# Kernel tuning notes

Hardware: AMD Instinct MI355X
Metric: run time of the kernel (lower is better)

The kernel has to match this reference:

```python
import jax, jax.numpy as jnp
import numpy as np

N = 197          # tokens (== token_count)
B = 64           # batch
D = 768          # d_model
NH = 12          # n_head
GH = 2           # global_heads
HR = NH // GH    # head_ratio = 6
DH = 64          # d_head
QK = GH * DH     # qk_dim = 128
ML = 3           # mask_levels
EPS = 1e-5


def setup_inputs() -> dict:
    key = jax.random.key(0)
    ks = jax.random.split(key, 9)
    s = 1.0 / np.sqrt(D)
    return {
        "h": jax.random.normal(ks[0], (N, B, D), dtype=jnp.float32),
        "masks": jax.random.uniform(ks[1], (N, N, ML), dtype=jnp.float32),
        "Wq": jax.random.normal(ks[2], (QK, D), dtype=jnp.float32) * s,
        "Wk": jax.random.normal(ks[3], (QK, D), dtype=jnp.float32) * s,
        "Wv": jax.random.normal(ks[4], (NH * DH, D), dtype=jnp.float32) * s,
        "Wo": jax.random.normal(ks[5], (D, NH * DH), dtype=jnp.float32) * s,
        "mask_proj": jnp.ones((ML, NH), dtype=jnp.float32),
        "ln_gamma": jnp.ones((D,), dtype=jnp.float32),
        "ln_beta": jnp.zeros((D,), dtype=jnp.float32),
    }


def reference(h, masks, Wq, Wk, Wv, Wo, mask_proj, ln_gamma, ln_beta):
    scale = 1.0 / np.sqrt(DH)
    # projections (seq-first layout [N, B, ...])
    q = (h @ Wq.T).reshape(N, B, GH, DH)
    k = (h @ Wk.T).reshape(N, B, GH, DH)
    v = (h @ Wv.T).reshape(N, B, NH, DH)
    # global-head scores: [B, GH, i, j]
    score = jnp.einsum('ibgd,jbgd->bgij', q, k) * scale
    # learned mask mix: [i, j, NH] -> [GH, i, j, HR] (g-major head split, matches torch reshape)
    mw = jnp.einsum('ijl,ln->ijn', masks, mask_proj)
    mw = mw.reshape(N, N, GH, HR).transpose(2, 0, 1, 3)
    # broadcast each global head to HR local heads: [B, GH, i, j, HR]
    attn = score[..., None] * mw[None]
    attn = attn.transpose(0, 1, 4, 2, 3).reshape(B, NH, N, N)  # head = g*HR + r
    prob = jax.nn.softmax(attn, axis=-1)
    # AV: [i, B, NH, DH] -> [N, B, NH*DH]
    vec = jnp.einsum('bnij,jbnd->ibnd', prob, v).reshape(N, B, NH * DH)
    out = vec @ Wo.T
    # post-LN residual
    x = h + out
    mu = jnp.mean(x, axis=-1, keepdims=True)
    var = jnp.var(x, axis=-1, keepdims=True)
    return ln_gamma * (x - mu) / jnp.sqrt(var + EPS) + ln_beta
```

## Files before the change

kernel.cpp:

```cpp
#include <hip/hip_runtime.h>
#include <hip/hip_bf16.h>
#include <stdint.h>

#define NTOK 197
#define NPAD 224
#define BATCH 64
#define DMODEL 768
#define NHEAD 12
#define GHEAD 2
#define HRATIO 6
#define DHEAD 64
#define QKDIM 128
#define LNEPS 1e-5f
#define MROWS (NTOK * BATCH)
#define MPAD 12672

using f32x4 = __attribute__((ext_vector_type(4))) float;
using s16x8 = __attribute__((ext_vector_type(8))) short;
using s16x4 = __attribute__((ext_vector_type(4))) short;

__device__ __forceinline__ short f2bf(float f) {
  unsigned int x = __float_as_uint(f);
  return (short)((x + 0x7fffu + ((x >> 16) & 1u)) >> 16);
}

__device__ __forceinline__ void gld16(void* lds, const void* g) {
  __builtin_amdgcn_global_load_lds(
      (const __attribute__((address_space(1))) unsigned int*)g,
      (__attribute__((address_space(3))) unsigned int*)lds, 16, 0, 0);
}

#define NB_H 4728
#define NB_QKV 384
#define NB_WO 288
__global__ __launch_bounds__(256)
void prep_kernel(const float* __restrict__ h, const float* __restrict__ Wq,
                 const float* __restrict__ Wk, const float* __restrict__ Wv,
                 const float* __restrict__ Wo, short* __restrict__ hb,
                 short* __restrict__ Wqkvb, short* __restrict__ Wob) {
  const int bb = blockIdx.x, t = threadIdx.x;
  const float* src;
  short* dst;
  if (bb < NB_H) {
    int idx = bb * 256 + t;
    src = h + (size_t)idx * 8;
    dst = hb + (size_t)idx * 8;
  } else if (bb < NB_H + NB_QKV) {
    int idx = (bb - NB_H) * 256 + t;
    int r = idx / 96, u = idx - r * 96;
    const float* s0 = (r < 128) ? Wq + (size_t)r * DMODEL
                    : (r < 256) ? Wk + (size_t)(r - 128) * DMODEL
                                : Wv + (size_t)(r - 256) * DMODEL;
    src = s0 + u * 8;
    dst = Wqkvb + (size_t)r * DMODEL + u * 8;
  } else {
    int idx = (bb - NB_H - NB_QKV) * 256 + t;
    src = Wo + (size_t)idx * 8;
    dst = Wob + (size_t)idx * 8;
  }
  float4 a = *(const float4*)src;
  float4 c = *(const float4*)(src + 4);
  s16x8 o;
  o[0] = f2bf(a.x); o[1] = f2bf(a.y); o[2] = f2bf(a.z); o[3] = f2bf(a.w);
  o[4] = f2bf(c.x); o[5] = f2bf(c.y); o[6] = f2bf(c.z); o[7] = f2bf(c.w);
  *(s16x8*)dst = o;
}

template<int OUTMODE>
__global__ __launch_bounds__(256)
void gemm_bt_kernel(const short* __restrict__ A, const short* __restrict__ W,
                    const float* __restrict__ R, void* __restrict__ Cout,
                    int M, int K, int NC) {
  __shared__ short As[128 * 32];
  __shared__ short Ws[128 * 32];
  const int tid = threadIdx.x;
  const int bn = blockIdx.x * 128;
  const int bm = blockIdx.y * 128;
  const int w = tid >> 6, l = tid & 63;
  const int wr = w >> 1, wc = w & 1;
  const int lm = l & 15, lh = l >> 4;

  const int srow = tid >> 2;
  const int schunk = (tid & 3) ^ ((tid >> 3) & 3);
  const short* Ag = A + (size_t)(bm + srow) * K + schunk * 8;
  const short* Wg = W + (size_t)(bn + srow) * K + schunk * 8;

  const int csw = lh ^ ((lm >> 1) & 3);
  f32x4 acc[4][4] = {};

  for (int kt = 0; kt < K; kt += 32) {
    __syncthreads();
    gld16(As + tid * 8, Ag + kt);
    gld16(As + 2048 + tid * 8, Ag + (size_t)64 * K + kt);
    gld16(Ws + tid * 8, Wg + kt);
    gld16(Ws + 2048 + tid * 8, Wg + (size_t)64 * K + kt);
    __syncthreads();
    s16x8 af[4], bf[4];
#pragma unroll
    for (int m = 0; m < 4; ++m)
      af[m] = *(const s16x8*)((const char*)As + (wr * 64 + m * 16 + lm) * 64 + csw * 16);
#pragma unroll
    for (int n = 0; n < 4; ++n)
      bf[n] = *(const s16x8*)((const char*)Ws + (wc * 64 + n * 16 + lm) * 64 + csw * 16);
#pragma unroll
    for (int m = 0; m < 4; ++m)
#pragma unroll
      for (int n = 0; n < 4; ++n)
        acc[m][n] = __builtin_amdgcn_mfma_f32_16x16x32_bf16(af[m], bf[n], acc[m][n], 0, 0, 0);
  }

#pragma unroll
  for (int m = 0; m < 4; ++m) {
#pragma unroll
    for (int r = 0; r < 4; ++r) {
      int row = bm + wr * 64 + m * 16 + lh * 4 + r;
      if (row < M) {
        if (OUTMODE == 0) {
          short* Cb = (short*)Cout;
#pragma unroll
          for (int n = 0; n < 4; ++n) {
            int col = bn + wc * 64 + n * 16 + lm;
            Cb[(size_t)row * NC + col] = f2bf(acc[m][n][r]);
          }
        } else {
          float* Cf = (float*)Cout;
#pragma unroll
          for (int n = 0; n < 4; ++n) {
            int col = bn + wc * 64 + n * 16 + lm;
            size_t idx = (size_t)row * NC + col;
            Cf[idx] = acc[m][n][r] + R[idx];
          }
        }
      }
    }
  }
}

__global__ __launch_bounds__(256)
void packall_kernel(const short* __restrict__ Cb, const float* __restrict__ masks,
                    const float* __restrict__ mproj, short* __restrict__ qp,
                    short* __restrict__ kp, short* __restrict__ vT,
                    float* __restrict__ mwp) {
  __shared__ short Vs[NPAD][DHEAD + 1];
  const int bb = blockIdx.x, t = threadIdx.x;
  if (bb < 256) {
    int b = bb >> 2, g = (bb >> 1) & 1, which = bb & 1;
    short* dst = (which ? kp : qp) + ((size_t)b * GHEAD + g) * NPAD * 64;
    int d = t & 63, iofs = t >> 6;
    for (int i0 = 0; i0 < NPAD; i0 += 4) {
      int i = i0 + iofs;
      short v = 0;
      if (i < NTOK)
        v = Cb[(size_t)(i * BATCH + b) * 1024 + which * QKDIM + g * DHEAD + d];
      int dd = which ? ((((d >> 3) ^ (i & 7)) << 3) | (d & 7)) : d;
      dst[i * 64 + dd] = v;
    }
  } else if (bb < 1024) {
    int vv = bb - 256;
    int b = vv / 12, n = vv - b * 12;
    int d = t & 63, iofs = t >> 6;
    for (int i0 = 0; i0 < NPAD; i0 += 4) {
      int i = i0 + iofs;
      short v = 0;
      if (i < NTOK)
        v = Cb[(size_t)(i * BATCH + b) * 1024 + 256 + n * DHEAD + d];
      Vs[i][d] = v;
    }
    __syncthreads();
    short* dst = vT + ((size_t)b * NHEAD + n) * DHEAD * NPAD;
    int sub = t & 63, dr = t >> 6;
    for (int d0 = 0; d0 < DHEAD; d0 += 4) {
      if (sub < 56) {
        int dd = d0 + dr, j0 = sub * 4;
        s16x4 o;
        o[0] = Vs[j0][dd]; o[1] = Vs[j0 + 1][dd];
        o[2] = Vs[j0 + 2][dd]; o[3] = Vs[j0 + 3][dd];
        *(s16x4*)(dst + dd * NPAD + j0) = o;
      }
    }
  } else {
    int e = (bb - 1024) * 256 + t;
    int n = e >> 12;
    int rem = e & 4095;
    int i = rem >> 4, lm = rem & 15;
    float p0 = mproj[n], p1 = mproj[NHEAD + n], p2 = mproj[2 * NHEAD + n];
    float vals[16];
#pragma unroll
    for (int jf = 0; jf < 16; ++jf) vals[jf] = 0.f;
    if (i < NTOK) {
#pragma unroll
      for (int jf = 0; jf < 14; ++jf) {
        int col = jf * 16 + lm;
        if (col < NTOK) {
          const float* mp = masks + ((size_t)i * NTOK + col) * 3;
          vals[jf] = 0.125f * (mp[0] * p0 + mp[1] * p1 + mp[2] * p2);
        }
      }
    }
    float* dst = mwp + (size_t)e * 16;
#pragma unroll
    for (int q = 0; q < 4; ++q) {
      float4 o = make_float4(vals[q * 4], vals[q * 4 + 1], vals[q * 4 + 2], vals[q * 4 + 3]);
      *(float4*)(dst + q * 4) = o;
    }
  }
}

__global__ __launch_bounds__(256, 2)
void attn_fused_kernel(const short* __restrict__ qp, const short* __restrict__ kp,
                       const short* __restrict__ vT, const float* __restrict__ mwp,
                       short* __restrict__ vec_b) {
  const int it = blockIdx.x, b = blockIdx.y, g = blockIdx.z;
  __shared__ short Ks[NPAD * 64];
  __shared__ short Pt[64 * 256];
  __shared__ float rsb[64];
  const int t = threadIdx.x, w = t >> 6, l = t & 63;
  const int lm = l & 15, lh = l >> 4, l7 = l & 7;

  const short* qg = qp + ((size_t)b * GHEAD + g) * NPAD * 64;
  const short* kg = kp + ((size_t)b * GHEAD + g) * NPAD * 64;

#pragma unroll
  for (int s = 0; s < 7; ++s)
    gld16(Ks + s * 2048 + t * 8, kg + s * 2048 + t * 8);
  int qrow = it * 64 + w * 16 + lm;
  if (qrow > NPAD - 1) qrow = NPAD - 1;
  s16x8 a0 = *(const s16x8*)(qg + qrow * 64 + lh * 8);
  s16x8 a1 = *(const s16x8*)(qg + qrow * 64 + 32 + lh * 8);
  __syncthreads();

  f32x4 acc[14] = {};
#pragma unroll
  for (int jf = 0; jf < 14; ++jf) {
    s16x8 kf0 = *(const s16x8*)((const char*)Ks + (jf * 16 + lm) * 128 + ((lh ^ l7) << 4));
    s16x8 kf1 = *(const s16x8*)((const char*)Ks + (jf * 16 + lm) * 128 + (((4 + lh) ^ l7) << 4));
    acc[jf] = __builtin_amdgcn_mfma_f32_16x16x32_bf16(a0, kf0, acc[jf], 0, 0, 0);
    acc[jf] = __builtin_amdgcn_mfma_f32_16x16x32_bf16(a1, kf1, acc[jf], 0, 0, 0);
  }

  for (int hh = 0; hh < HRATIO; ++hh) {
    const int n = g * HRATIO + hh;
    const short* vg = vT + ((size_t)b * NHEAD + n) * 64 * NPAD;
    s16x8 vf[7];
#pragma unroll
    for (int ks = 0; ks < 7; ++ks)
      vf[ks] = *(const s16x8*)(vg + (w * 16 + lm) * NPAD + ks * 32 + lh * 8);

#pragma unroll
    for (int r = 0; r < 4; ++r) {
      const int row = w * 16 + lh * 4 + r;
      const int i = it * 64 + row;
      const float* mr = mwp + (((size_t)n * 256 + i) * 16 + lm) * 16;
      f32x4 mv0 = *(const f32x4*)(mr);
      f32x4 mv1 = *(const f32x4*)(mr + 4);
      f32x4 mv2 = *(const f32x4*)(mr + 8);
      f32x4 mv3 = *(const f32x4*)(mr + 12);
      float sum = 0.f;
#pragma unroll
      for (int jf = 0; jf < 13; ++jf) {
        float mwv = (jf < 4) ? mv0[jf] : (jf < 8) ? mv1[jf - 4]
                  : (jf < 12) ? mv2[jf - 8] : mv3[jf - 12];
        float pe = __expf(acc[jf][r] * mwv);
        if (jf == 12 && lm >= 5) pe = 0.f;
        sum += pe;
        int byteoff = row * 512 + (((2 * jf + (lm >> 3)) ^ (row & 7)) << 4) + (lm & 7) * 2;
        *(short*)((char*)Pt + byteoff) = f2bf(pe);
      }
      {
        int byteoff = row * 512 + (((26 + (lm >> 3)) ^ (row & 7)) << 4) + (lm & 7) * 2;
        *(short*)((char*)Pt + byteoff) = 0;
      }
#pragma unroll
      for (int off = 8; off; off >>= 1) sum += __shfl_xor(sum, off);
      if (lm == 0) rsb[row] = 1.f / sum;
    }
    __syncthreads();

    __builtin_amdgcn_s_setprio(1);
    f32x4 oacc[4] = {};
#pragma unroll
    for (int fi = 0; fi < 4; ++fi)
#pragma unroll
      for (int ks = 0; ks < 7; ++ks) {
        s16x8 pa = *(const s16x8*)((const char*)Pt + (fi * 16 + lm) * 512 +
                                   (((ks * 4 + lh) ^ l7) << 4));
        oacc[fi] = __builtin_amdgcn_mfma_f32_16x16x32_bf16(pa, vf[ks], oacc[fi], 0, 0, 0);
      }
    __builtin_amdgcn_s_setprio(0);
#pragma unroll
    for (int fi = 0; fi < 4; ++fi)
#pragma unroll
      for (int r = 0; r < 4; ++r) {
        int ia = it * 64 + fi * 16 + lh * 4 + r;
        if (ia < NTOK) {
          float rsv = rsb[fi * 16 + lh * 4 + r];
          vec_b[((size_t)ia * BATCH + b) * DMODEL + n * 64 + w * 16 + lm] =
              f2bf(oacc[fi][r] * rsv);
        }
      }
    __syncthreads();
  }
}

__global__ __launch_bounds__(256)
void ln_kernel(float* __restrict__ x, const float* __restrict__ gamma,
               const float* __restrict__ beta) {
  const int m = blockIdx.x;
  float* row = x + (size_t)m * DMODEL;
  const int tid = threadIdx.x;
  float v0 = row[tid], v1 = row[tid + 256], v2 = row[tid + 512];
  float s = v0 + v1 + v2;
  float sq = v0 * v0 + v1 * v1 + v2 * v2;
#pragma unroll
  for (int off = 32; off; off >>= 1) {
    s += __shfl_xor(s, off);
    sq += __shfl_xor(sq, off);
  }
  __shared__ float ss[4], ssq[4];
  const int w = tid >> 6, lane = tid & 63;
  if (lane == 0) { ss[w] = s; ssq[w] = sq; }
  __syncthreads();
  s = ss[0] + ss[1] + ss[2] + ss[3];
  sq = ssq[0] + ssq[1] + ssq[2] + ssq[3];
  const float inv = 1.0f / (float)DMODEL;
  float mu = s * inv;
  float var = sq * inv - mu * mu;
  float rstd = rsqrtf(var + LNEPS);
  row[tid] = gamma[tid] * (v0 - mu) * rstd + beta[tid];
  row[tid + 256] = gamma[tid + 256] * (v1 - mu) * rstd + beta[tid + 256];
  row[tid + 512] = gamma[tid + 512] * (v2 - mu) * rstd + beta[tid + 512];
}

extern "C" void kernel_launch(void* const* d_in, const int* in_sizes, int n_in,
                              void* d_out, int out_size, void* d_ws, size_t ws_size,
                              hipStream_t stream) {
  const float* h     = (const float*)d_in[0];
  const float* masks = (const float*)d_in[1];
  const float* Wq    = (const float*)d_in[2];
  const float* Wk    = (const float*)d_in[3];
  const float* Wv    = (const float*)d_in[4];
  const float* Wo    = (const float*)d_in[5];
  const float* mproj = (const float*)d_in[6];
  const float* gamma = (const float*)d_in[7];
  const float* beta  = (const float*)d_in[8];
  float* out = (float*)d_out;

  char* ws = (char*)d_ws;
  size_t o = 0;
  auto alloc = [&](size_t bytes) { size_t r = o; o += (bytes + 255) & ~(size_t)255; return r; };
  short* hb    = (short*)(ws + alloc((size_t)MPAD * DMODEL * 2));
  short* Cb    = (short*)(ws + alloc((size_t)MPAD * 1024 * 2));
  short* Wqkvb = (short*)(ws + alloc((size_t)1024 * DMODEL * 2));
  short* Wob   = (short*)(ws + alloc((size_t)DMODEL * DMODEL * 2));
  short* qp    = (short*)(ws + alloc((size_t)BATCH * GHEAD * NPAD * DHEAD * 2));
  short* kp    = (short*)(ws + alloc((size_t)BATCH * GHEAD * NPAD * DHEAD * 2));
  short* vT    = (short*)(ws + alloc((size_t)BATCH * NHEAD * DHEAD * NPAD * 2));
  float* mwp   = (float*)(ws + alloc((size_t)NHEAD * 256 * 16 * 16 * 4));
  short* vec_b = hb;

  prep_kernel<<<NB_H + NB_QKV + NB_WO, 256, 0, stream>>>(h, Wq, Wk, Wv, Wo, hb, Wqkvb, Wob);
  gemm_bt_kernel<0><<<dim3(1024 / 128, MPAD / 128), 256, 0, stream>>>(
      hb, Wqkvb, nullptr, Cb, MROWS, DMODEL, 1024);
  packall_kernel<<<1216, 256, 0, stream>>>(Cb, masks, mproj, qp, kp, vT, mwp);
  attn_fused_kernel<<<dim3(4, BATCH, GHEAD), 256, 0, stream>>>(qp, kp, vT, mwp, vec_b);
  gemm_bt_kernel<1><<<dim3(DMODEL / 128, MPAD / 128), 256, 0, stream>>>(
      vec_b, Wob, h, out, MROWS, DMODEL, DMODEL);
  ln_kernel<<<MROWS, 256, 0, stream>>>(out, gamma, beta);
}
```

Measured before the change: 166.8 us.

## Write output projection as bf16 and fuse residual add into LayerNorm; remap GEMM blocks per XCD

After: 156.0 us. 1.07x faster.

```diff
diff --git a/kernel.cpp b/kernel.cpp
--- a/kernel.cpp
+++ b/kernel.cpp
@@ -22,6 +22,10 @@
 __device__ __forceinline__ short f2bf(float f) {
   unsigned int x = __float_as_uint(f);
   return (short)((x + 0x7fffu + ((x >> 16) & 1u)) >> 16);
+}
+
+__device__ __forceinline__ float bf2f(short s) {
+  return __uint_as_float((unsigned)(unsigned short)s << 16);
 }
 
 __device__ __forceinline__ void gld16(void* lds, const void* g) {
@@ -66,16 +70,21 @@
   *(s16x8*)dst = o;
 }
 
-template<int OUTMODE>
 __global__ __launch_bounds__(256)
 void gemm_bt_kernel(const short* __restrict__ A, const short* __restrict__ W,
-                    const float* __restrict__ R, void* __restrict__ Cout,
-                    int M, int K, int NC) {
+                    short* __restrict__ Cout, int M, int K, int NC) {
   __shared__ short As[128 * 32];
   __shared__ short Ws[128 * 32];
   const int tid = threadIdx.x;
-  const int bn = blockIdx.x * 128;
-  const int bm = blockIdx.y * 128;
+
+  const int nwg = gridDim.x * gridDim.y;
+  const int orig = blockIdx.y * gridDim.x + blockIdx.x;
+  const int qq = nwg >> 3, rr = nwg & 7;
+  const int xcd = orig & 7, sidx = orig >> 3;
+  const int wg = (xcd < rr ? xcd * (qq + 1) : rr * (qq + 1) + (xcd - rr) * qq) + sidx;
+  const int bn = (wg % gridDim.x) * 128;
+  const int bm = (wg / gridDim.x) * 128;
+
   const int w = tid >> 6, l = tid & 63;
   const int wr = w >> 1, wc = w & 1;
   const int lm = l & 15, lh = l >> 4;
@@ -115,21 +124,10 @@
     for (int r = 0; r < 4; ++r) {
       int row = bm + wr * 64 + m * 16 + lh * 4 + r;
       if (row < M) {
-        if (OUTMODE == 0) {
-          short* Cb = (short*)Cout;
-#pragma unroll
-          for (int n = 0; n < 4; ++n) {
-            int col = bn + wc * 64 + n * 16 + lm;
-            Cb[(size_t)row * NC + col] = f2bf(acc[m][n][r]);
-          }
-        } else {
-          float* Cf = (float*)Cout;
-#pragma unroll
-          for (int n = 0; n < 4; ++n) {
-            int col = bn + wc * 64 + n * 16 + lm;
-            size_t idx = (size_t)row * NC + col;
-            Cf[idx] = acc[m][n][r] + R[idx];
-          }
+#pragma unroll
+        for (int n = 0; n < 4; ++n) {
+          int col = bn + wc * 64 + n * 16 + lm;
+          Cout[(size_t)row * NC + col] = f2bf(acc[m][n][r]);
         }
       }
     }
@@ -303,12 +301,17 @@
 }
 
 __global__ __launch_bounds__(256)
-void ln_kernel(float* __restrict__ x, const float* __restrict__ gamma,
+void ln_kernel(const float* __restrict__ h, const short* __restrict__ proj_b,
+               float* __restrict__ out, const float* __restrict__ gamma,
                const float* __restrict__ beta) {
   const int m = blockIdx.x;
-  float* row = x + (size_t)m * DMODEL;
+  const float* hrow = h + (size_t)m * DMODEL;
+  const short* prow = proj_b + (size_t)m * DMODEL;
+  float* orow = out + (size_t)m * DMODEL;
   const int tid = threadIdx.x;
-  float v0 = row[tid], v1 = row[tid + 256], v2 = row[tid + 512];
+  float v0 = hrow[tid] + bf2f(prow[tid]);
+  float v1 = hrow[tid + 256] + bf2f(prow[tid + 256]);
+  float v2 = hrow[tid + 512] + bf2f(prow[tid + 512]);
   float s = v0 + v1 + v2;
   float sq = v0 * v0 + v1 * v1 + v2 * v2;
 #pragma unroll
@@ -326,9 +329,9 @@
   float mu = s * inv;
   float var = sq * inv - mu * mu;
   float rstd = rsqrtf(var + LNEPS);
-  row[tid] = gamma[tid] * (v0 - mu) * rstd + beta[tid];
-  row[tid + 256] = gamma[tid + 256] * (v1 - mu) * rstd + beta[tid + 256];
-  row[tid + 512] = gamma[tid + 512] * (v2 - mu) * rstd + beta[tid + 512];
+  orow[tid] = gamma[tid] * (v0 - mu) * rstd + beta[tid];
+  orow[tid + 256] = gamma[tid + 256] * (v1 - mu) * rstd + beta[tid + 256];
+  orow[tid + 512] = gamma[tid + 512] * (v2 - mu) * rstd + beta[tid + 512];
 }
 
 extern "C" void kernel_launch(void* const* d_in, const int* in_sizes, int n_in,
@@ -357,13 +360,14 @@
   short* vT    = (short*)(ws + alloc((size_t)BATCH * NHEAD * DHEAD * NPAD * 2));
   float* mwp   = (float*)(ws + alloc((size_t)NHEAD * 256 * 16 * 16 * 4));
   short* vec_b = hb;
+  short* proj_b = Cb;
 
   prep_kernel<<<NB_H + NB_QKV + NB_WO, 256, 0, stream>>>(h, Wq, Wk, Wv, Wo, hb, Wqkvb, Wob);
-  gemm_bt_kernel<0><<<dim3(1024 / 128, MPAD / 128), 256, 0, stream>>>(
-      hb, Wqkvb, nullptr, Cb, MROWS, DMODEL, 1024);
+  gemm_bt_kernel<<<dim3(1024 / 128, MPAD / 128), 256, 0, stream>>>(
+      hb, Wqkvb, Cb, MROWS, DMODEL, 1024);
   packall_kernel<<<1216, 256, 0, stream>>>(Cb, masks, mproj, qp, kp, vT, mwp);
   attn_fused_kernel<<<dim3(4, BATCH, GHEAD), 256, 0, stream>>>(qp, kp, vT, mwp, vec_b);
-  gemm_bt_kernel<1><<<dim3(DMODEL / 128, MPAD / 128), 256, 0, stream>>>(
-      vec_b, Wob, h, out, MROWS, DMODEL, DMODEL);
-  ln_kernel<<<MROWS, 256, 0, stream>>>(out, gamma, beta);
-}
+  gemm_bt_kernel<<<dim3(DMODEL / 128, MPAD / 128), 256, 0, stream>>>(
+      vec_b, Wob, proj_b, MROWS, DMODEL, DMODEL);
+  ln_kernel<<<MROWS, 256, 0, stream>>>(h, proj_b, out, gamma, beta);
+}
```
